# Kernel optimization log

Measured on AMD Instinct MI355X. Metric: run time of the kernel, lower is better.

The kernel has to match this reference:

```python
import jax, jax.numpy as jnp
import numpy as np

N_NODES = 2048
N_ATTRS = 64
TOP_K = 8


def setup_inputs() -> dict:
    key = jax.random.key(0)
    kx, ka = jax.random.split(key)
    x = jax.random.normal(kx, (N_NODES, N_ATTRS), dtype=jnp.float32)
    adj = jax.random.uniform(ka, (N_NODES, N_NODES), dtype=jnp.float32)
    return {"x": x, "adj": adj, "k": TOP_K}


def reference(x, adj, k):
    # h[j, f, i] = adj[i, j] * x[i, f]: contribution of source node i's
    # attribute f to destination node j, weighted by edge (i -> j).
    # Matches TF: expand/broadcast then transpose(2,1,0).
    h = adj.T[:, None, :] * x.T[None, :, :]          # (N, F, N)
    topk_vals = jax.lax.top_k(h, k)[0]               # (N, F, K), sorted desc
    out = jnp.concatenate([x[:, :, None], topk_vals], axis=-1)  # (N, F, K+1)
    return jnp.transpose(out, (0, 2, 1))             # (N, K+1, F)
```

## Files before the change

kernel.cpp:

```cpp
#include <hip/hip_runtime.h>
#include <hip/hip_bf16.h>
#include <math.h>

#define NN 2048
#define NF 64
#define KK 8
#define C  16

__device__ float    g_xs[NF * NN];
__device__ unsigned g_xi[NF * NN];
__device__ float    g_sm[NF * NN];

__global__ __launch_bounds__(1024)
void order_kernel(const float* __restrict__ x) {
  __shared__ int   hist[256];
  __shared__ int   scan[256];
  __shared__ int   offs[256];
  __shared__ float svals[NN];
  const int f = blockIdx.x;
  const int tid = threadIdx.x;

  if (tid < 256) hist[tid] = 0;
  __syncthreads();

  float v0 = x[(size_t)tid * NF + f];
  float v1 = x[(size_t)(tid + 1024) * NF + f];
  int b0 = (int)((3.6f - v0) * 35.4f); b0 = b0 < 0 ? 0 : (b0 > 255 ? 255 : b0);
  int b1 = (int)((3.6f - v1) * 35.4f); b1 = b1 < 0 ? 0 : (b1 > 255 ? 255 : b1);
  atomicAdd(&hist[b0], 1);
  atomicAdd(&hist[b1], 1);
  __syncthreads();

  if (tid < 256) scan[tid] = hist[tid];
  __syncthreads();
  for (int d = 1; d < 256; d <<= 1) {
    int o = 0;
    if (tid < 256 && tid >= d) o = scan[tid - d];
    __syncthreads();
    if (tid < 256) scan[tid] += o;
    __syncthreads();
  }
  if (tid < 256) offs[tid] = scan[tid] - hist[tid];
  __syncthreads();

  int p0 = atomicAdd(&offs[b0], 1);
  int p1 = atomicAdd(&offs[b1], 1);
  svals[p0] = v0;
  svals[p1] = v1;
  g_xs[f * NN + p0] = v0;  g_xi[f * NN + p0] = (unsigned)tid;
  g_xs[f * NN + p1] = v1;  g_xi[f * NN + p1] = (unsigned)(tid + 1024);
  __syncthreads();

  for (int d = 1; d < NN; d <<= 1) {
    float o0 = (tid + d < NN) ? svals[tid + d] : -INFINITY;
    float o1 = (tid + 1024 + d < NN) ? svals[tid + 1024 + d] : -INFINITY;
    __syncthreads();
    svals[tid]        = fmaxf(svals[tid], o0);
    svals[tid + 1024] = fmaxf(svals[tid + 1024], o1);
    __syncthreads();
  }
  g_sm[f * NN + tid]        = svals[tid];
  g_sm[f * NN + tid + 1024] = svals[tid + 1024];
}

__device__ __forceinline__ void ins8(float (&t)[KK], float p) {
  t[7] = fmaxf(t[7], p);
#pragma unroll
  for (int s = KK - 1; s >= 1; --s) {
    float hi = fmaxf(t[s - 1], t[s]);
    float lo = fminf(t[s - 1], t[s]);
    t[s - 1] = hi;
    t[s] = lo;
  }
}

__global__ __launch_bounds__(512)
void topk_kernel(const float* __restrict__ x, const float* __restrict__ adj,
                 float* __restrict__ out) {
  const int tid  = threadIdx.x;
  const int lane = tid & 63;
  const int w    = tid >> 6;
  const int jt   = blockIdx.x & 31;
  const int fg   = blockIdx.x >> 5;
  const int f    = (fg << 3) + w;
  const int j    = (jt << 6) + lane;

  const float*    vp = g_xs + f * NN;
  const unsigned* ip = g_xi + f * NN;
  const float*    sp = g_sm + f * NN;

  float t8[KK];
#pragma unroll
  for (int s = 0; s < KK; ++s) t8[s] = -INFINITY;

  int t = 0;
  for (;;) {
    const float4* vp4 = (const float4*)(vp + t);
    const uint4*  ip4 = (const uint4*)(ip + t);
    float4 xv4[4];
    uint4  xi4[4];
#pragma unroll
    for (int q = 0; q < 4; ++q) { xv4[q] = vp4[q]; xi4[q] = ip4[q]; }

    float a[C];
#pragma unroll
    for (int q = 0; q < 4; ++q) {
      a[q * 4 + 0] = adj[((size_t)xi4[q].x << 11) + j];
      a[q * 4 + 1] = adj[((size_t)xi4[q].y << 11) + j];
      a[q * 4 + 2] = adj[((size_t)xi4[q].z << 11) + j];
      a[q * 4 + 3] = adj[((size_t)xi4[q].w << 11) + j];
    }
#pragma unroll
    for (int q = 0; q < 4; ++q) {
      ins8(t8, a[q * 4 + 0] * xv4[q].x);
      ins8(t8, a[q * 4 + 1] * xv4[q].y);
      ins8(t8, a[q * 4 + 2] * xv4[q].z);
      ins8(t8, a[q * 4 + 3] * xv4[q].w);
    }

    t += C;
    if (t >= NN) break;
    float bound = fmaxf(sp[t], 0.0f);
    if (__all(t8[KK - 1] >= bound)) break;
  }

  __shared__ float obuf[KK + 1][64][8];
  obuf[0][lane][w] = x[(size_t)j * NF + f];
#pragma unroll
  for (int s = 0; s < KK; ++s) obuf[s + 1][lane][w] = t8[s];
  __syncthreads();

  const int f0 = fg << 3;
  for (int r = tid; r < (KK + 1) * 64 * 2; r += 512) {
    int rs  = r >> 7;
    int rem = r & 127;
    int rj  = rem >> 1;
    int h   = rem & 1;
    float4 v = make_float4(obuf[rs][rj][h * 4 + 0], obuf[rs][rj][h * 4 + 1],
                           obuf[rs][rj][h * 4 + 2], obuf[rs][rj][h * 4 + 3]);
    *(float4*)(out + (size_t)((jt << 6) + rj) * ((KK + 1) * NF) +
               rs * NF + f0 + (h << 2)) = v;
  }
}

extern "C" void kernel_launch(void* const* d_in, const int* in_sizes, int n_in,
                              void* d_out, int out_size, void* d_ws, size_t ws_size,
                              hipStream_t stream) {
  const float* x   = (const float*)d_in[0];
  const float* adj = (const float*)d_in[1];
  float* out = (float*)d_out;
  hipLaunchKernelGGL(order_kernel, dim3(NF), dim3(1024), 0, stream, x);
  hipLaunchKernelGGL(topk_kernel, dim3(256), dim3(512), 0, stream, x, adj, out);
}
```

Before: 88.20 us.

## Split each feature's candidate scan across two waves with double-buffered gathers

```diff
diff --git a/kernel.cpp b/kernel.cpp
--- a/kernel.cpp
+++ b/kernel.cpp
@@ -5,13 +5,12 @@
 #define NN 2048
 #define NF 64
 #define KK 8
-#define C  16
 
 __device__ float    g_xs[NF * NN];
 __device__ unsigned g_xi[NF * NN];
 __device__ float    g_sm[NF * NN];
 
-__global__ __launch_bounds__(1024)
+__global__ __launch_bounds__(256)
 void order_kernel(const float* __restrict__ x) {
   __shared__ int   hist[256];
   __shared__ int   scan[256];
@@ -20,47 +19,62 @@
   const int f = blockIdx.x;
   const int tid = threadIdx.x;
 
-  if (tid < 256) hist[tid] = 0;
-  __syncthreads();
-
-  float v0 = x[(size_t)tid * NF + f];
-  float v1 = x[(size_t)(tid + 1024) * NF + f];
-  int b0 = (int)((3.6f - v0) * 35.4f); b0 = b0 < 0 ? 0 : (b0 > 255 ? 255 : b0);
-  int b1 = (int)((3.6f - v1) * 35.4f); b1 = b1 < 0 ? 0 : (b1 > 255 ? 255 : b1);
-  atomicAdd(&hist[b0], 1);
-  atomicAdd(&hist[b1], 1);
-  __syncthreads();
-
-  if (tid < 256) scan[tid] = hist[tid];
+  hist[tid] = 0;
+  __syncthreads();
+
+  float v[8];
+  int   b[8];
+#pragma unroll
+  for (int k = 0; k < 8; ++k) {
+    int e = tid + (k << 8);
+    v[k] = x[(size_t)e * NF + f];
+    int bb = (int)((3.6f - v[k]) * 35.4f);
+    b[k] = bb < 0 ? 0 : (bb > 255 ? 255 : bb);
+    atomicAdd(&hist[b[k]], 1);
+  }
+  __syncthreads();
+
+  scan[tid] = hist[tid];
   __syncthreads();
   for (int d = 1; d < 256; d <<= 1) {
-    int o = 0;
-    if (tid < 256 && tid >= d) o = scan[tid - d];
-    __syncthreads();
-    if (tid < 256) scan[tid] += o;
-    __syncthreads();
-  }
-  if (tid < 256) offs[tid] = scan[tid] - hist[tid];
-  __syncthreads();
-
-  int p0 = atomicAdd(&offs[b0], 1);
-  int p1 = atomicAdd(&offs[b1], 1);
-  svals[p0] = v0;
-  svals[p1] = v1;
-  g_xs[f * NN + p0] = v0;  g_xi[f * NN + p0] = (unsigned)tid;
-  g_xs[f * NN + p1] = v1;  g_xi[f * NN + p1] = (unsigned)(tid + 1024);
+    int o = (tid >= d) ? scan[tid - d] : 0;
+    __syncthreads();
+    scan[tid] += o;
+    __syncthreads();
+  }
+  offs[tid] = scan[tid] - hist[tid];
+  __syncthreads();
+
+#pragma unroll
+  for (int k = 0; k < 8; ++k) {
+    int e = tid + (k << 8);
+    int p = atomicAdd(&offs[b[k]], 1);
+    svals[p] = v[k];
+    g_xs[f * NN + p] = v[k];
+    g_xi[f * NN + p] = (unsigned)e;
+  }
   __syncthreads();
 
   for (int d = 1; d < NN; d <<= 1) {
-    float o0 = (tid + d < NN) ? svals[tid + d] : -INFINITY;
-    float o1 = (tid + 1024 + d < NN) ? svals[tid + 1024 + d] : -INFINITY;
-    __syncthreads();
-    svals[tid]        = fmaxf(svals[tid], o0);
-    svals[tid + 1024] = fmaxf(svals[tid + 1024], o1);
-    __syncthreads();
-  }
-  g_sm[f * NN + tid]        = svals[tid];
-  g_sm[f * NN + tid + 1024] = svals[tid + 1024];
+    float o[8];
+#pragma unroll
+    for (int k = 0; k < 8; ++k) {
+      int p = tid + (k << 8);
+      o[k] = (p + d < NN) ? svals[p + d] : -INFINITY;
+    }
+    __syncthreads();
+#pragma unroll
+    for (int k = 0; k < 8; ++k) {
+      int p = tid + (k << 8);
+      svals[p] = fmaxf(svals[p], o[k]);
+    }
+    __syncthreads();
+  }
+#pragma unroll
+  for (int k = 0; k < 8; ++k) {
+    int p = tid + (k << 8);
+    g_sm[f * NN + p] = svals[p];
+  }
 }
 
 __device__ __forceinline__ void ins8(float (&t)[KK], float p) {
@@ -74,15 +88,50 @@
   }
 }
 
-__global__ __launch_bounds__(512)
+struct Buf {
+  float4 v0, v1;
+  uint4  i0, i1;
+  float  a[8];
+};
+
+__device__ __forceinline__ void loadc(Buf& B, const float* vp, const unsigned* ip,
+                                      const float* __restrict__ adj, int j, int pos) {
+  B.v0 = *(const float4*)(vp + pos);
+  B.v1 = *(const float4*)(vp + pos + 4);
+  B.i0 = *(const uint4*)(ip + pos);
+  B.i1 = *(const uint4*)(ip + pos + 4);
+  B.a[0] = adj[((size_t)B.i0.x << 11) + j];
+  B.a[1] = adj[((size_t)B.i0.y << 11) + j];
+  B.a[2] = adj[((size_t)B.i0.z << 11) + j];
+  B.a[3] = adj[((size_t)B.i0.w << 11) + j];
+  B.a[4] = adj[((size_t)B.i1.x << 11) + j];
+  B.a[5] = adj[((size_t)B.i1.y << 11) + j];
+  B.a[6] = adj[((size_t)B.i1.z << 11) + j];
+  B.a[7] = adj[((size_t)B.i1.w << 11) + j];
+}
+
+__device__ __forceinline__ void proc(const Buf& B, float (&t8)[KK]) {
+  ins8(t8, B.a[0] * B.v0.x);
+  ins8(t8, B.a[1] * B.v0.y);
+  ins8(t8, B.a[2] * B.v0.z);
+  ins8(t8, B.a[3] * B.v0.w);
+  ins8(t8, B.a[4] * B.v1.x);
+  ins8(t8, B.a[5] * B.v1.y);
+  ins8(t8, B.a[6] * B.v1.z);
+  ins8(t8, B.a[7] * B.v1.w);
+}
+
+__global__ __launch_bounds__(512, 4)
 void topk_kernel(const float* __restrict__ x, const float* __restrict__ adj,
                  float* __restrict__ out) {
   const int tid  = threadIdx.x;
   const int lane = tid & 63;
-  const int w    = tid >> 6;
+  const int w    = __builtin_amdgcn_readfirstlane(tid >> 6);
+  const int ff   = w >> 1;
+  const int h    = w & 1;
   const int jt   = blockIdx.x & 31;
   const int fg   = blockIdx.x >> 5;
-  const int f    = (fg << 3) + w;
+  const int f    = (fg << 2) + ff;
   const int j    = (jt << 6) + lane;
 
   const float*    vp = g_xs + f * NN;
@@ -93,53 +142,52 @@
 #pragma unroll
   for (int s = 0; s < KK; ++s) t8[s] = -INFINITY;
 
-  int t = 0;
+  Buf A, B;
+  int t = h << 3;
+  loadc(A, vp, ip, adj, j, t);
   for (;;) {
-    const float4* vp4 = (const float4*)(vp + t);
-    const uint4*  ip4 = (const uint4*)(ip + t);
-    float4 xv4[4];
-    uint4  xi4[4];
-#pragma unroll
-    for (int q = 0; q < 4; ++q) { xv4[q] = vp4[q]; xi4[q] = ip4[q]; }
-
-    float a[C];
-#pragma unroll
-    for (int q = 0; q < 4; ++q) {
-      a[q * 4 + 0] = adj[((size_t)xi4[q].x << 11) + j];
-      a[q * 4 + 1] = adj[((size_t)xi4[q].y << 11) + j];
-      a[q * 4 + 2] = adj[((size_t)xi4[q].z << 11) + j];
-      a[q * 4 + 3] = adj[((size_t)xi4[q].w << 11) + j];
-    }
-#pragma unroll
-    for (int q = 0; q < 4; ++q) {
-      ins8(t8, a[q * 4 + 0] * xv4[q].x);
-      ins8(t8, a[q * 4 + 1] * xv4[q].y);
-      ins8(t8, a[q * 4 + 2] * xv4[q].z);
-      ins8(t8, a[q * 4 + 3] * xv4[q].w);
-    }
-
-    t += C;
-    if (t >= NN) break;
-    float bound = fmaxf(sp[t], 0.0f);
-    if (__all(t8[KK - 1] >= bound)) break;
-  }
-
-  __shared__ float obuf[KK + 1][64][8];
-  obuf[0][lane][w] = x[(size_t)j * NF + f];
-#pragma unroll
-  for (int s = 0; s < KK; ++s) obuf[s + 1][lane][w] = t8[s];
-  __syncthreads();
-
-  const int f0 = fg << 3;
-  for (int r = tid; r < (KK + 1) * 64 * 2; r += 512) {
-    int rs  = r >> 7;
-    int rem = r & 127;
-    int rj  = rem >> 1;
-    int h   = rem & 1;
-    float4 v = make_float4(obuf[rs][rj][h * 4 + 0], obuf[rs][rj][h * 4 + 1],
-                           obuf[rs][rj][h * 4 + 2], obuf[rs][rj][h * 4 + 3]);
+    int tn = t + 16;
+    bool hn = tn < NN;
+    if (hn) loadc(B, vp, ip, adj, j, tn);
+    proc(A, t8);
+    if (!hn) break;
+    if (__all(t8[KK - 1] >= fmaxf(sp[tn], 0.0f))) break;
+    t = tn;
+    tn = t + 16;
+    hn = tn < NN;
+    if (hn) loadc(A, vp, ip, adj, j, tn);
+    proc(B, t8);
+    if (!hn) break;
+    if (__all(t8[KK - 1] >= fmaxf(sp[tn], 0.0f))) break;
+    t = tn;
+  }
+
+  __shared__ float part[4][2][KK][64];
+  __shared__ float obuf[KK + 1][64][4];
+#pragma unroll
+  for (int s = 0; s < KK; ++s) part[ff][h][s][lane] = t8[s];
+  __syncthreads();
+
+  if (tid < 256) {
+    const int jl = tid & 63;
+    const int fl = tid >> 6;
+    float best[KK];
+#pragma unroll
+    for (int s = 0; s < KK; ++s) best[s] = part[fl][0][s][jl];
+#pragma unroll
+    for (int s = 0; s < KK; ++s) ins8(best, part[fl][1][s][jl]);
+    obuf[0][jl][fl] = x[(size_t)((jt << 6) + jl) * NF + (fg << 2) + fl];
+#pragma unroll
+    for (int s = 0; s < KK; ++s) obuf[s + 1][jl][fl] = best[s];
+  }
+  __syncthreads();
+
+  for (int r = tid; r < 64 * (KK + 1); r += 512) {
+    int rj = r / (KK + 1);
+    int rs = r - rj * (KK + 1);
+    float4 vv = *(const float4*)&obuf[rs][rj][0];
     *(float4*)(out + (size_t)((jt << 6) + rj) * ((KK + 1) * NF) +
-               rs * NF + f0 + (h << 2)) = v;
+               rs * NF + (fg << 2)) = vv;
   }
 }
 
@@ -149,6 +197,6 @@
   const float* x   = (const float*)d_in[0];
   const float* adj = (const float*)d_in[1];
   float* out = (float*)d_out;
-  hipLaunchKernelGGL(order_kernel, dim3(NF), dim3(1024), 0, stream, x);
-  hipLaunchKernelGGL(topk_kernel, dim3(256), dim3(512), 0, stream, x, adj, out);
-}
+  hipLaunchKernelGGL(order_kernel, dim3(NF), dim3(256), 0, stream, x);
+  hipLaunchKernelGGL(topk_kernel, dim3(512), dim3(512), 0, stream, x, adj, out);
+}
```

Measured after the change: 94.95 us. 1.08x slower.
